# Kernel optimization log

Measured on AMD Instinct MI355X. Metric: run time of the kernel, lower is better.

Reference implementation:

```python
import jax, jax.numpy as jnp
import numpy as np

DILATIONS = (1, 2, 4, 8, 16, 32, 64, 128, 256, 512)
K = 3            # kernel_size
CH = 128         # channels
B, T = 4, 16384
L = len(DILATIONS)


def _conv1x1(x, w, b=None):
    # x: [B, Cin, T], w: [Cout, Cin, 1] -> [B, Cout, T]
    y = jnp.einsum('oc,bct->bot', w[..., 0], x)
    return y if b is None else y + b[None, :, None]


def _causal_dilated_conv(x, w, b, d):
    # buffer of zeros of size (K-1)*d concatenated on the left == causal left pad
    pad = (K - 1) * d
    y = jax.lax.conv_general_dilated(
        x, w, window_strides=(1,), padding=[(pad, 0)], rhs_dilation=(d,),
        dimension_numbers=('NCH', 'OIH', 'NCH'))
    return y + b[None, :, None]


def setup_inputs() -> dict:
    key = jax.random.key(0)
    ks = jax.random.split(key, 12)
    s = 0.1  # keep gated activations out of saturation
    return {
        'x': jax.random.normal(ks[0], (B, 1, T), jnp.float32),
        'c': jax.random.normal(ks[1], (B, 1, T), jnp.float32),
        'head_init': jnp.zeros((B, CH, T), jnp.float32),
        'w_re': jax.random.normal(ks[2], (CH, 1, 1), jnp.float32) * s,
        'conv_w': jax.random.normal(ks[3], (L, 2 * CH, CH, K), jnp.float32) * s,
        'conv_b': jax.random.normal(ks[4], (L, 2 * CH), jnp.float32) * s,
        'mix_w': jax.random.normal(ks[5], (L, 2 * CH, 1, 1), jnp.float32) * s,
        'w1x1': jax.random.normal(ks[6], (L, CH, CH, 1), jnp.float32) * s,
        'b1x1': jax.random.normal(ks[7], (L, CH), jnp.float32) * s,
        'w_head': jax.random.normal(ks[8], (1, CH, 1), jnp.float32) * s,
        'b_head': jax.random.normal(ks[9], (1,), jnp.float32) * s,
    }


def reference(x, c, head_init, w_re, conv_w, conv_b, mix_w, w1x1, b1x1, w_head, b_head):
    h = _conv1x1(x, w_re)               # rechannel: [B, CH, T]
    head = head_init                    # head accumulator (zeros == head_input=None)
    for li, d in enumerate(DILATIONS):  # fixed small layer loop (structurally distinct dilations)
        z = _causal_dilated_conv(h, conv_w[li], conv_b[li], d)   # [B, 2CH, T]
        z = z + _conv1x1(c, mix_w[li])                           # conditioning mixer
        post = jnp.tanh(z[:, :CH]) * jax.nn.sigmoid(z[:, CH:])   # gated activation
        h = h + _conv1x1(post, w1x1[li], b1x1[li])               # residual
        head = head + post
    out = _conv1x1(head, w_head, b_head)  # [B, 1, T]
    return out, h
```

## Files before the change

### kernel.cpp

```cpp
#include <hip/hip_runtime.h>
#include <hip/hip_bf16.h>

#define B_   4
#define T_   16384
#define CH_  128
#define TCH_ 256
#define NL_  10
#define TT_  64
#define SHW_ 196

typedef __attribute__((ext_vector_type(8))) short short8;
typedef __attribute__((ext_vector_type(16))) float f32x16;

#define MFMA32(a, b, c) __builtin_amdgcn_mfma_f32_32x32x16_bf16(a, b, c, 0, 0, 0)

__device__ __forceinline__ unsigned short f2bf(float f) {
  unsigned u = __float_as_uint(f);
  return (unsigned short)((u + 0x7FFFu + ((u >> 16) & 1u)) >> 16);
}
__device__ __forceinline__ unsigned pk2bf(float lo, float hi) {
  unsigned r;
  asm("v_cvt_pk_bf16_f32 %0, %1, %2" : "=v"(r) : "v"(lo), "v"(hi));
  return r;
}
__device__ __forceinline__ float bf2f(unsigned s) {
  return __uint_as_float((s & 0xFFFFu) << 16);
}
__device__ __forceinline__ float fast_tanh(float x) {
  float e = __expf(2.0f * fabsf(x));
  float t = 1.0f - 2.0f / (e + 1.0f);
  return copysignf(t, x);
}
__device__ __forceinline__ float fast_sig(float x) {
  return 1.0f / (1.0f + __expf(-x));
}

__global__ __launch_bounds__(256) void prep_k(
    const float* __restrict__ conv_w, const float* __restrict__ w1x1,
    unsigned short* __restrict__ wpackA, unsigned short* __restrict__ wpack1,
    const float* __restrict__ x, const float* __restrict__ w_re,
    unsigned short* __restrict__ hb,
    const float* __restrict__ head_init, const float* __restrict__ w_head,
    const float* __restrict__ b_head, float* __restrict__ out) {
  const unsigned bid = blockIdx.x;
  if (bid < 4480u) {
    const int NA = NL_ * 8 * 24 * 64 * 8;
    int idx = bid * 256 + threadIdx.x;
    if (idx < NA) {
      int j = idx & 7;
      int l = (idx >> 3) & 63;
      int t2 = idx >> 9;
      int ks = t2 % 24;
      int t3 = t2 / 24;
      int of = t3 & 7;
      int li = t3 >> 3;
      int o = 32 * of + (l & 31);
      int ck = 16 * ks + 8 * (l >> 5) + j;
      int c = ck & 127, ktap = ck >> 7;
      wpackA[idx] = f2bf(conv_w[((li * TCH_ + o) * CH_ + c) * 3 + ktap]);
    } else {
      int i2 = idx - NA;
      if (i2 < NL_ * 4 * 8 * 64 * 8) {
        int j = i2 & 7;
        int l = (i2 >> 3) & 63;
        int ks = (i2 >> 9) & 7;
        int of = (i2 >> 12) & 3;
        int li = i2 >> 14;
        int o = 32 * of + (l & 31);
        int c = 16 * ks + 8 * (l >> 5) + j;
        wpack1[i2] = f2bf(w1x1[(li * CH_ + o) * CH_ + c]);
      }
    }
  } else if (bid < 8576u) {
    int flat = (bid - 4480u) * 256 + threadIdx.x;
    int cid = flat & 15;
    int t = (flat >> 4) & (T_ - 1);
    int b = flat >> 18;
    float xv = x[b * T_ + t];
    const float* wr = w_re + cid * 8;
    union { short8 s; unsigned short u[8]; } o;
#pragma unroll
    for (int j = 0; j < 8; ++j) o.u[j] = f2bf(wr[j] * xv);
    *(short8*)(hb + (size_t)(b * T_ + t) * CH_ + cid * 8) = o.s;
  } else {
    int idx = (bid - 8576u) * 256 + threadIdx.x;
    int b = idx / T_;
    int t = idx - b * T_;
    float acc = b_head[0];
#pragma unroll 8
    for (int c = 0; c < CH_; ++c)
      acc += w_head[c] * head_init[(b * CH_ + c) * T_ + t];
    out[idx] = acc;
  }
}

__global__ __launch_bounds__(256, 3) void layer_k(
    const unsigned short* __restrict__ hin,
    unsigned short* __restrict__ hob,
    float* __restrict__ hof,
    const float* __restrict__ cin, float* __restrict__ out,
    const unsigned short* __restrict__ wA,
    const unsigned short* __restrict__ w1p,
    const float* __restrict__ bconv,
    const float* __restrict__ wmix,
    const float* __restrict__ b1,
    const float* __restrict__ w_head,
    int d, int is_final) {
  __shared__ unsigned shH[TT_ * SHW_];
  __shared__ float shR[4 * 64];

  const int tid = threadIdx.x;
  const int b = blockIdx.y;
  const int tile = (blockIdx.x & 7) * 32 + (blockIdx.x >> 3);
  const int t0 = tile * TT_;

#pragma unroll
  for (int it = 0; it < 12; ++it) {
    int flat = it * 256 + tid;
    int cid = flat & 15;
    int tt = (flat >> 4) & 63;
    int k = flat >> 10;
    int t = t0 + tt - (2 - k) * d;
    uint4 v = make_uint4(0u, 0u, 0u, 0u);
    if (t >= 0)
      v = *(const uint4*)(hin + ((size_t)(b * T_ + t) * CH_ + cid * 8));
    *(uint4*)(shH + tt * SHW_ + k * 64 + cid * 4) = v;
  }
  __syncthreads();

  const int wave = __builtin_amdgcn_readfirstlane(tid >> 6);
  const int lane = tid & 63;
  const int ln = lane & 31;
  const int kg = lane >> 5;

  f32x16 aL0, aL1, aH0, aH1;
#pragma unroll
  for (int i = 0; i < 16; ++i) { aL0[i] = 0.f; aL1[i] = 0.f; aH0[i] = 0.f; aH1[i] = 0.f; }

  const short8* wAv = (const short8*)wA;
#pragma unroll
  for (int ks = 0; ks < 24; ++ks) {
    short8 b0 = *(const short8*)(shH + ln * SHW_ + 8 * ks + 4 * kg);
    short8 b1f = *(const short8*)(shH + (32 + ln) * SHW_ + 8 * ks + 4 * kg);
    short8 alo = wAv[(wave * 24 + ks) * 64 + lane];
    short8 ahi = wAv[((wave + 4) * 24 + ks) * 64 + lane];
    aL0 = MFMA32(alo, b0, aL0);
    aL1 = MFMA32(alo, b1f, aL1);
    aH0 = MFMA32(ahi, b0, aH0);
    aH1 = MFMA32(ahi, b1f, aH1);
  }
  __syncthreads();

  const float cq0 = cin[b * T_ + t0 + ln];
  const float cq1 = cin[b * T_ + t0 + 32 + ln];
  float hs0 = 0.f, hs1 = 0.f;
#pragma unroll
  for (int r2 = 0; r2 < 4; ++r2) {
    const int o4 = 32 * wave + 8 * r2 + 4 * kg;
    const float4 bcL = *(const float4*)(bconv + o4);
    const float4 bcH = *(const float4*)(bconv + CH_ + o4);
    const float4 wmL = *(const float4*)(wmix + o4);
    const float4 wmH = *(const float4*)(wmix + CH_ + o4);
    const float4 wh = *(const float4*)(w_head + o4);
    float pv0[4], pv1[4];
#pragma unroll
    for (int j2 = 0; j2 < 4; ++j2) {
      const float bl = ((const float*)&bcL)[j2], bh = ((const float*)&bcH)[j2];
      const float ml = ((const float*)&wmL)[j2], mh = ((const float*)&wmH)[j2];
      const float w = ((const float*)&wh)[j2];
      float zl0 = aL0[4 * r2 + j2] + bl + ml * cq0;
      float zh0 = aH0[4 * r2 + j2] + bh + mh * cq0;
      pv0[j2] = fast_tanh(zl0) * fast_sig(zh0);
      hs0 += w * pv0[j2];
      float zl1 = aL1[4 * r2 + j2] + bl + ml * cq1;
      float zh1 = aH1[4 * r2 + j2] + bh + mh * cq1;
      pv1[j2] = fast_tanh(zl1) * fast_sig(zh1);
      hs1 += w * pv1[j2];
    }
    uint2 pk;
    const int dw = 16 * wave + 4 * r2 + 2 * kg;
    pk.x = pk2bf(pv0[0], pv0[1]);
    pk.y = pk2bf(pv0[2], pv0[3]);
    *(uint2*)(shH + ln * SHW_ + dw) = pk;
    pk.x = pk2bf(pv1[0], pv1[1]);
    pk.y = pk2bf(pv1[2], pv1[3]);
    *(uint2*)(shH + (32 + ln) * SHW_ + dw) = pk;
  }
  hs0 += __shfl_xor(hs0, 32);
  hs1 += __shfl_xor(hs1, 32);
  if (lane < 32) {
    shR[wave * 64 + ln] = hs0;
    shR[wave * 64 + 32 + ln] = hs1;
  }
  __syncthreads();

  f32x16 d0, d1;
#pragma unroll
  for (int i = 0; i < 16; ++i) { d0[i] = 0.f; d1[i] = 0.f; }

  const short8* w1v = (const short8*)w1p;
#pragma unroll
  for (int ks = 0; ks < 8; ++ks) {
    short8 p0 = *(const short8*)(shH + ln * SHW_ + 8 * ks + 4 * kg);
    short8 p1 = *(const short8*)(shH + (32 + ln) * SHW_ + 8 * ks + 4 * kg);
    short8 a = w1v[(wave * 8 + ks) * 64 + lane];
    d0 = MFMA32(a, p0, d0);
    d1 = MFMA32(a, p1, d1);
  }

  if (tid < 64) {
    float tot = shR[tid] + shR[64 + tid] + shR[128 + tid] + shR[192 + tid];
    out[b * T_ + t0 + tid] += tot;
  }

  float res0[16], res1[16];
#pragma unroll
  for (int r2 = 0; r2 < 4; ++r2) {
    const int o4 = 32 * wave + 8 * r2 + 4 * kg;
    const float4 b14 = *(const float4*)(b1 + o4);
    const int dw = 16 * wave + 4 * r2 + 2 * kg;
    uint2 h0 = *(const uint2*)(shH + ln * SHW_ + 128 + dw);
    uint2 h1 = *(const uint2*)(shH + (32 + ln) * SHW_ + 128 + dw);
    res0[4 * r2 + 0] = bf2f(h0.x) + ((const float*)&b14)[0] + d0[4 * r2 + 0];
    res0[4 * r2 + 1] = bf2f(h0.x >> 16) + ((const float*)&b14)[1] + d0[4 * r2 + 1];
    res0[4 * r2 + 2] = bf2f(h0.y) + ((const float*)&b14)[2] + d0[4 * r2 + 2];
    res0[4 * r2 + 3] = bf2f(h0.y >> 16) + ((const float*)&b14)[3] + d0[4 * r2 + 3];
    res1[4 * r2 + 0] = bf2f(h1.x) + ((const float*)&b14)[0] + d1[4 * r2 + 0];
    res1[4 * r2 + 1] = bf2f(h1.x >> 16) + ((const float*)&b14)[1] + d1[4 * r2 + 1];
    res1[4 * r2 + 2] = bf2f(h1.y) + ((const float*)&b14)[2] + d1[4 * r2 + 2];
    res1[4 * r2 + 3] = bf2f(h1.y >> 16) + ((const float*)&b14)[3] + d1[4 * r2 + 3];
  }

  if (!is_final) {
    __syncthreads();
#pragma unroll
    for (int r2 = 0; r2 < 4; ++r2) {
      const int dw = 16 * wave + 4 * r2 + 2 * kg;
      uint2 pk;
      pk.x = pk2bf(res0[4 * r2 + 0], res0[4 * r2 + 1]);
      pk.y = pk2bf(res0[4 * r2 + 2], res0[4 * r2 + 3]);
      *(uint2*)(shH + ln * SHW_ + dw) = pk;
      pk.x = pk2bf(res1[4 * r2 + 0], res1[4 * r2 + 1]);
      pk.y = pk2bf(res1[4 * r2 + 2], res1[4 * r2 + 3]);
      *(uint2*)(shH + (32 + ln) * SHW_ + dw) = pk;
    }
    __syncthreads();
#pragma unroll
    for (int it = 0; it < 4; ++it) {
      int flat = it * 256 + tid;
      int cid = flat & 15;
      int tt = flat >> 4;
      *(uint4*)(hob + ((size_t)(b * T_ + t0 + tt) * CH_ + cid * 8)) =
          *(const uint4*)(shH + tt * SHW_ + cid * 4);
    }
  } else {
#pragma unroll
    for (int r2 = 0; r2 < 4; ++r2) {
#pragma unroll
      for (int j2 = 0; j2 < 4; ++j2) {
        const int o = 32 * wave + 8 * r2 + 4 * kg + j2;
        hof[(size_t)(b * CH_ + o) * T_ + t0 + ln] = res0[4 * r2 + j2];
        hof[(size_t)(b * CH_ + o) * T_ + t0 + 32 + ln] = res1[4 * r2 + j2];
      }
    }
  }
}

extern "C" void kernel_launch(void* const* d_in, const int* in_sizes, int n_in,
                              void* d_out, int out_size, void* d_ws, size_t ws_size,
                              hipStream_t stream) {
  const float* x         = (const float*)d_in[0];
  const float* c         = (const float*)d_in[1];
  const float* head_init = (const float*)d_in[2];
  const float* w_re      = (const float*)d_in[3];
  const float* conv_w    = (const float*)d_in[4];
  const float* conv_b    = (const float*)d_in[5];
  const float* mix_w     = (const float*)d_in[6];
  const float* w1x1      = (const float*)d_in[7];
  const float* b1x1      = (const float*)d_in[8];
  const float* w_head    = (const float*)d_in[9];
  const float* b_head    = (const float*)d_in[10];

  float* out = (float*)d_out;
  float* hof = out + B_ * T_;

  unsigned short* hb0 = (unsigned short*)d_ws;
  unsigned short* hb1 = hb0 + (size_t)B_ * T_ * CH_;
  unsigned short* wpackA = hb1 + (size_t)B_ * T_ * CH_;
  unsigned short* wpack1 = wpackA + NL_ * 8 * 24 * 64 * 8;

  prep_k<<<8832, 256, 0, stream>>>(conv_w, w1x1, wpackA, wpack1,
                                   x, w_re, hb0,
                                   head_init, w_head, b_head, out);

  const int dil[NL_] = {1, 2, 4, 8, 16, 32, 64, 128, 256, 512};
  for (int li = 0; li < NL_; ++li) {
    const unsigned short* hin = (li & 1) ? hb1 : hb0;
    unsigned short* hob       = (li & 1) ? hb0 : hb1;
    int is_final = (li == NL_ - 1);
    layer_k<<<dim3(T_ / TT_, B_), 256, 0, stream>>>(
        hin, hob, hof, c, out,
        wpackA + li * (8 * 24 * 64 * 8),
        wpack1 + li * (4 * 8 * 64 * 8),
        conv_b + li * TCH_,
        mix_w + li * TCH_,
        b1x1 + li * CH_,
        w_head,
        dil[li], is_final);
  }
}
```

Measured before the change: 308.6 us.

## Process two time tiles per block with register-prefetched second tile

Each layer block now handles two consecutive 64-step tiles instead of one, halving the grid. The second tile's dilated input rows are loaded into registers before the first tile is computed, then written to LDS after it, so the global-load latency is hidden behind the first tile's MFMA work. Launch bounds drop from 3 to 2 blocks per CU to make room for the 12 extra uint4 registers, which lowers occupancy and leaves fewer blocks (512) to spread across CUs.

```diff
diff --git a/kernel.cpp b/kernel.cpp
--- a/kernel.cpp
+++ b/kernel.cpp
@@ -94,40 +94,14 @@
   }
 }
 
-__global__ __launch_bounds__(256, 3) void layer_k(
-    const unsigned short* __restrict__ hin,
-    unsigned short* __restrict__ hob,
-    float* __restrict__ hof,
+__device__ __forceinline__ void tile_body(
+    int b, int t0, int is_final,
+    unsigned short* __restrict__ hob, float* __restrict__ hof,
     const float* __restrict__ cin, float* __restrict__ out,
-    const unsigned short* __restrict__ wA,
-    const unsigned short* __restrict__ w1p,
-    const float* __restrict__ bconv,
-    const float* __restrict__ wmix,
-    const float* __restrict__ b1,
-    const float* __restrict__ w_head,
-    int d, int is_final) {
-  __shared__ unsigned shH[TT_ * SHW_];
-  __shared__ float shR[4 * 64];
-
-  const int tid = threadIdx.x;
-  const int b = blockIdx.y;
-  const int tile = (blockIdx.x & 7) * 32 + (blockIdx.x >> 3);
-  const int t0 = tile * TT_;
-
-#pragma unroll
-  for (int it = 0; it < 12; ++it) {
-    int flat = it * 256 + tid;
-    int cid = flat & 15;
-    int tt = (flat >> 4) & 63;
-    int k = flat >> 10;
-    int t = t0 + tt - (2 - k) * d;
-    uint4 v = make_uint4(0u, 0u, 0u, 0u);
-    if (t >= 0)
-      v = *(const uint4*)(hin + ((size_t)(b * T_ + t) * CH_ + cid * 8));
-    *(uint4*)(shH + tt * SHW_ + k * 64 + cid * 4) = v;
-  }
-  __syncthreads();
-
+    const short8* __restrict__ wAv, const short8* __restrict__ w1v,
+    const float* __restrict__ bconv, const float* __restrict__ wmix,
+    const float* __restrict__ b1, const float* __restrict__ w_head,
+    unsigned* shH, float* shR, int tid) {
   const int wave = __builtin_amdgcn_readfirstlane(tid >> 6);
   const int lane = tid & 63;
   const int ln = lane & 31;
@@ -137,7 +111,6 @@
 #pragma unroll
   for (int i = 0; i < 16; ++i) { aL0[i] = 0.f; aL1[i] = 0.f; aH0[i] = 0.f; aH1[i] = 0.f; }
 
-  const short8* wAv = (const short8*)wA;
 #pragma unroll
   for (int ks = 0; ks < 24; ++ks) {
     short8 b0 = *(const short8*)(shH + ln * SHW_ + 8 * ks + 4 * kg);
@@ -198,7 +171,6 @@
 #pragma unroll
   for (int i = 0; i < 16; ++i) { d0[i] = 0.f; d1[i] = 0.f; }
 
-  const short8* w1v = (const short8*)w1p;
 #pragma unroll
   for (int ks = 0; ks < 8; ++ks) {
     short8 p0 = *(const short8*)(shH + ln * SHW_ + 8 * ks + 4 * kg);
@@ -266,6 +238,76 @@
   }
 }
 
+__global__ __launch_bounds__(256, 2) void layer_k(
+    const unsigned short* __restrict__ hin,
+    unsigned short* __restrict__ hob,
+    float* __restrict__ hof,
+    const float* __restrict__ cin, float* __restrict__ out,
+    const unsigned short* __restrict__ wA,
+    const unsigned short* __restrict__ w1p,
+    const float* __restrict__ bconv,
+    const float* __restrict__ wmix,
+    const float* __restrict__ b1,
+    const float* __restrict__ w_head,
+    int d, int is_final) {
+  __shared__ unsigned shH[TT_ * SHW_];
+  __shared__ float shR[4 * 64];
+
+  const int tid = threadIdx.x;
+  const int b = blockIdx.y;
+  const int m = (blockIdx.x & 7) * 16 + (blockIdx.x >> 3);
+  const int t0A = (2 * m) * TT_;
+  const int t0B = t0A + TT_;
+
+  const short8* wAv = (const short8*)wA;
+  const short8* w1v = (const short8*)w1p;
+
+#pragma unroll
+  for (int it = 0; it < 12; ++it) {
+    int flat = it * 256 + tid;
+    int cid = flat & 15;
+    int tt = (flat >> 4) & 63;
+    int k = flat >> 10;
+    int t = t0A + tt - (2 - k) * d;
+    uint4 v = make_uint4(0u, 0u, 0u, 0u);
+    if (t >= 0)
+      v = *(const uint4*)(hin + ((size_t)(b * T_ + t) * CH_ + cid * 8));
+    *(uint4*)(shH + tt * SHW_ + k * 64 + cid * 4) = v;
+  }
+
+  uint4 vB[12];
+#pragma unroll
+  for (int it = 0; it < 12; ++it) {
+    int flat = it * 256 + tid;
+    int cid = flat & 15;
+    int tt = (flat >> 4) & 63;
+    int k = flat >> 10;
+    int t = t0B + tt - (2 - k) * d;
+    vB[it] = make_uint4(0u, 0u, 0u, 0u);
+    if (t >= 0)
+      vB[it] = *(const uint4*)(hin + ((size_t)(b * T_ + t) * CH_ + cid * 8));
+  }
+  __syncthreads();
+
+  tile_body(b, t0A, is_final, hob, hof, cin, out, wAv, w1v, bconv, wmix, b1,
+            w_head, shH, shR, tid);
+
+  __syncthreads();
+
+#pragma unroll
+  for (int it = 0; it < 12; ++it) {
+    int flat = it * 256 + tid;
+    int cid = flat & 15;
+    int tt = (flat >> 4) & 63;
+    int k = flat >> 10;
+    *(uint4*)(shH + tt * SHW_ + k * 64 + cid * 4) = vB[it];
+  }
+  __syncthreads();
+
+  tile_body(b, t0B, is_final, hob, hof, cin, out, wAv, w1v, bconv, wmix, b1,
+            w_head, shH, shR, tid);
+}
+
 extern "C" void kernel_launch(void* const* d_in, const int* in_sizes, int n_in,
                               void* d_out, int out_size, void* d_ws, size_t ws_size,
                               hipStream_t stream) {
@@ -298,7 +340,7 @@
     const unsigned short* hin = (li & 1) ? hb1 : hb0;
     unsigned short* hob       = (li & 1) ? hb0 : hb1;
     int is_final = (li == NL_ - 1);
-    layer_k<<<dim3(T_ / TT_, B_), 256, 0, stream>>>(
+    layer_k<<<dim3(128, B_), 256, 0, stream>>>(
         hin, hob, hof, c, out,
         wpackA + li * (8 * 24 * 64 * 8),
         wpack1 + li * (4 * 8 * 64 * 8),
```

New measurement: 313.6 us. No clear change (+1.6%).
